# Optimization experiments

Hardware: AMD Instinct MI355X
Metric: run time of the kernel (lower is better)

## Reference

```python
import jax, jax.numpy as jnp
import numpy as np

N = 100_000      # nodes
E = 1_600_000    # edges (avg degree 16)
IN, H, OUT = 960, 192, 3
NB = 6           # block_num


def setup_inputs() -> dict:
    key = jax.random.key(0)
    ks = jax.random.split(key, 14)
    s = 0.05  # weight init scale
    x = jax.random.normal(ks[0], (N, IN), jnp.float32)
    src = jax.random.randint(ks[1], (E,), 0, N, jnp.int32)
    dst = jax.random.randint(ks[2], (E,), 0, N, jnp.int32)
    # normalized adjacency values (like D^-1 A entries)
    ew = jax.random.uniform(ks[3], (E,), jnp.float32) / 16.0
    w1 = jax.random.normal(ks[4], (IN, H), jnp.float32) * s
    l1 = jax.random.normal(ks[5], (IN, H), jnp.float32) * s
    b1 = jnp.zeros((H,), jnp.float32)
    wb = jax.random.normal(ks[6], (2 * NB, H, H), jnp.float32) * s
    lb = jax.random.normal(ks[7], (2 * NB, H, H), jnp.float32) * s
    bb = jnp.zeros((2 * NB, H), jnp.float32)
    w2 = jax.random.normal(ks[8], (H, OUT), jnp.float32) * s
    l2 = jax.random.normal(ks[9], (H, OUT), jnp.float32) * s
    b2 = jnp.zeros((OUT,), jnp.float32)
    return dict(x=x, src=src, dst=dst, ew=ew, w1=w1, l1=l1, b1=b1,
                wb=wb, lb=lb, bb=bb, w2=w2, l2=l2, b2=b2)


def reference(x, src, dst, ew, w1, l1, b1, wb, lb, bb, w2, l2, b2):
    def gcn(h, w, lw, b):
        # GraphConvolution: spmm(adj, h @ w) + h @ loop_w + b
        sup = h @ w                                   # [N, F_out]
        msg = sup[src] * ew[:, None]                  # gather + weight  [E, F_out]
        agg = jax.ops.segment_sum(msg, dst, num_segments=N)
        return agg + h @ lw + b

    h = gcn(x, w1, l1, b1)                            # conv1: in_dim -> hidden
    for i in range(NB):                               # GResBlocks
        a = gcn(h, wb[2 * i], lb[2 * i], bb[2 * i])
        a = gcn(a, wb[2 * i + 1], lb[2 * i + 1], bb[2 * i + 1])
        h = (h + a) * 0.5                             # residual scaling
    x_cat = h
    x_out = gcn(x_cat, w2, l2, b2)                    # conv2: hidden -> out_dim
    return (x_out, x_cat)
```

## Files before the change

kernel.cpp:

```cpp
#include <hip/hip_runtime.h>

typedef __attribute__((ext_vector_type(8))) short short8;
typedef __attribute__((ext_vector_type(4))) float f32x4;
typedef __attribute__((ext_vector_type(4))) int int4v;
typedef __attribute__((ext_vector_type(2))) unsigned int u32x2;

__device__ __forceinline__ float bf2f(unsigned short u) {
  return __uint_as_float(((unsigned)u) << 16);
}
__device__ __forceinline__ unsigned short f2bf(float f) {
  unsigned u = __float_as_uint(f);
  return (unsigned short)((u + 0x7FFFu + ((u >> 16) & 1u)) >> 16);
}

#define GLB_CAST(p) ((const __attribute__((address_space(1))) void*)(p))
#define LDS_CAST(p) ((__attribute__((address_space(3))) void*)(p))

__global__ void count_kernel(const int* __restrict__ dst, int* __restrict__ cnt, int E) {
  int e = blockIdx.x * blockDim.x + threadIdx.x;
  if (e < E) atomicAdd(&cnt[dst[e] + 1], 1);
}

__global__ __launch_bounds__(256) void scan_bsum_kernel(const int* __restrict__ cnt,
                                                        int* __restrict__ bsum, int n) {
  __shared__ int buf[256];
  int tid = threadIdx.x;
  int j0 = blockIdx.x * 1024 + tid * 4;
  int s = 0;
#pragma unroll
  for (int k = 0; k < 4; k++) {
    int j = j0 + k;
    if (j < n) s += cnt[j];
  }
  buf[tid] = s;
  __syncthreads();
  for (int off = 128; off > 0; off >>= 1) {
    if (tid < off) buf[tid] += buf[tid + off];
    __syncthreads();
  }
  if (tid == 0) bsum[blockIdx.x] = buf[0];
}

__global__ __launch_bounds__(256) void scan_small_kernel(const int* __restrict__ bsum,
                                                         int* __restrict__ boff, int nb) {
  __shared__ int buf[2][256];
  int tid = threadIdx.x;
  int C = (nb + 255) >> 8;
  int start = tid * C;
  int end = start + C; if (end > nb) end = nb;
  int s = 0;
  for (int j = start; j < end; j++) s += bsum[j];
  buf[0][tid] = s;
  __syncthreads();
  int pin = 0;
  for (int off = 1; off < 256; off <<= 1) {
    int v = buf[pin][tid];
    if (tid >= off) v += buf[pin][tid - off];
    buf[pin ^ 1][tid] = v;
    pin ^= 1;
    __syncthreads();
  }
  int run = (tid == 0) ? 0 : buf[pin][tid - 1];
  for (int j = start; j < end; j++) {
    boff[j] = run;
    run += bsum[j];
  }
}

__global__ __launch_bounds__(256) void scan_final_kernel(const int* __restrict__ cnt,
                                                         const int* __restrict__ boff,
                                                         int* __restrict__ rowptr,
                                                         int* __restrict__ cur,
                                                         int n, int nrows) {
  __shared__ int buf[2][256];
  int tid = threadIdx.x;
  int j0 = blockIdx.x * 1024 + tid * 4;
  int v[4];
  int s = 0;
#pragma unroll
  for (int k = 0; k < 4; k++) {
    int j = j0 + k;
    v[k] = (j < n) ? cnt[j] : 0;
    s += v[k];
  }
  buf[0][tid] = s;
  __syncthreads();
  int pin = 0;
  for (int off = 1; off < 256; off <<= 1) {
    int t = buf[pin][tid];
    if (tid >= off) t += buf[pin][tid - off];
    buf[pin ^ 1][tid] = t;
    pin ^= 1;
    __syncthreads();
  }
  int run = boff[blockIdx.x] + ((tid == 0) ? 0 : buf[pin][tid - 1]);
#pragma unroll
  for (int k = 0; k < 4; k++) {
    int j = j0 + k;
    if (j < n) {
      run += v[k];
      rowptr[j] = run;
      if (j < nrows) cur[j] = run;
    }
  }
}

__global__ void fill_kernel(const int* __restrict__ src, const int* __restrict__ dst,
                            const float* __restrict__ ew,
                            int* __restrict__ cur, int2* __restrict__ s_edge, int E) {
  int e = blockIdx.x * blockDim.x + threadIdx.x;
  if (e >= E) return;
  int r = dst[e];
  int pos = atomicAdd(&cur[r], 1);
  s_edge[pos] = make_int2(src[e], __float_as_int(ew[e]));
}

__global__ void prep_w_kernel(const float* __restrict__ w1,
                              const float* __restrict__ l1,
                              const float* __restrict__ wb,
                              const float* __restrict__ lb,
                              unsigned short* __restrict__ Wt1,
                              unsigned short* __restrict__ Wtb) {
  int tid = blockIdx.x * blockDim.x + threadIdx.x;
  const int n1 = 384 * 960;
  const int nb = 12 * 384 * 192;
  if (tid < n1) {
    int c = tid / 960, k = tid % 960;
    Wt1[tid] = f2bf((c < 192) ? w1[k * 192 + c] : l1[k * 192 + (c - 192)]);
  } else if (tid < n1 + nb) {
    int u = tid - n1;
    int i = u / (384 * 192);
    int r = u % (384 * 192);
    int c = r / 192, k = r % 192;
    Wtb[u] = f2bf((c < 192) ? wb[(i * 192 + k) * 192 + c]
                            : lb[(i * 192 + k) * 192 + (c - 192)]);
  }
}

__device__ __forceinline__ short8 cvt_f32x8(const float* p) {
  f32x4 a = *reinterpret_cast<const f32x4*>(p);
  f32x4 b = *reinterpret_cast<const f32x4*>(p + 4);
  short8 r;
  r[0] = (short)f2bf(a[0]); r[1] = (short)f2bf(a[1]);
  r[2] = (short)f2bf(a[2]); r[3] = (short)f2bf(a[3]);
  r[4] = (short)f2bf(b[0]); r[5] = (short)f2bf(b[1]);
  r[6] = (short)f2bf(b[2]); r[7] = (short)f2bf(b[3]);
  return r;
}

__global__ __launch_bounds__(512) void gemm_f32_kernel(const float* __restrict__ A,
                                                       const unsigned short* __restrict__ Wt,
                                                       unsigned short* __restrict__ out,
                                                       int nrows, int K) {
  __shared__ char lds_raw[40960];

  int tid = threadIdx.x;
  int lane = tid & 63;
  int w = tid >> 6;
  int rg = w >> 1, ch = w & 1;
  int row0blk = blockIdx.x * 256;
  int row0 = row0blk + rg * 64;
  int l15 = lane & 15, lq = lane >> 4;

  f32x4 acc[12][4];
#pragma unroll
  for (int cf = 0; cf < 12; cf++)
#pragma unroll
    for (int rf = 0; rf < 4; rf++) acc[cf][rf] = (f32x4)(0.0f);

  int tiles = K / 32;
  for (int tile = 0; tile < tiles; ++tile) {
    __syncthreads();
#pragma unroll
    for (int it = 0; it < 3; ++it) {
      int slot = it * 512 + tid;
      int q = slot / 384, c = slot - q * 384;
      const unsigned short* g = Wt + (size_t)c * K + tile * 32 + q * 8;
      __builtin_amdgcn_global_load_lds(GLB_CAST(g), LDS_CAST(lds_raw + 16384 + slot * 16), 16, 0, 0);
    }
#pragma unroll
    for (int it = 0; it < 2; ++it) {
      int slot = it * 512 + tid;
      int c = slot >> 8, row = slot & 255;
      int grow = row0blk + row;
      if (grow > nrows - 1) grow = nrows - 1;
      const float* g = A + (size_t)grow * K + tile * 32 + c * 8;
      *reinterpret_cast<short8*>(lds_raw + slot * 16) = cvt_f32x8(g);
    }
    __syncthreads();

    short8 af[4];
#pragma unroll
    for (int rf = 0; rf < 4; rf++)
      af[rf] = *reinterpret_cast<const short8*>(
          lds_raw + lq * 4096 + (rg * 64 + rf * 16 + l15) * 16);
#pragma unroll
    for (int cf = 0; cf < 12; cf++) {
      const short8 bf = *reinterpret_cast<const short8*>(
          lds_raw + 16384 + (lq * 384 + ch * 192 + cf * 16 + l15) * 16);
#pragma unroll
      for (int rf = 0; rf < 4; rf++)
        acc[cf][rf] = __builtin_amdgcn_mfma_f32_16x16x32_bf16(bf, af[rf], acc[cf][rf], 0, 0, 0);
    }
  }

#pragma unroll
  for (int rf = 0; rf < 4; rf++) {
    int row = row0 + rf * 16 + l15;
    if (row >= nrows) continue;
    unsigned short* orow = out + (size_t)row * 384 + ch * 192 + lq * 4;
#pragma unroll
    for (int cf = 0; cf < 12; cf++) {
      u32x2 pv;
      pv[0] = (unsigned)f2bf(acc[cf][rf][0]) | ((unsigned)f2bf(acc[cf][rf][1]) << 16);
      pv[1] = (unsigned)f2bf(acc[cf][rf][2]) | ((unsigned)f2bf(acc[cf][rf][3]) << 16);
      *reinterpret_cast<u32x2*>(orow + cf * 16) = pv;
    }
  }
}

__global__ __launch_bounds__(512) void gemm_bf16_db_kernel(const unsigned short* __restrict__ A,
                                                           const unsigned short* __restrict__ Wt,
                                                           unsigned short* __restrict__ out,
                                                           int nrows, int K) {
  extern __shared__ char lds_db[];

  int tid = threadIdx.x;
  int lane = tid & 63;
  int w = tid >> 6;
  int rg = w >> 1, ch = w & 1;
  int row0blk = blockIdx.x * 256;
  int row0 = row0blk + rg * 64;
  int l15 = lane & 15, lq = lane >> 4;

  f32x4 acc[12][4];
#pragma unroll
  for (int cf = 0; cf < 12; cf++)
#pragma unroll
    for (int rf = 0; rf < 4; rf++) acc[cf][rf] = (f32x4)(0.0f);

  auto stage = [&](int tile, int buf) {
    char* base = lds_db + buf * 40960;
#pragma unroll
    for (int it = 0; it < 3; ++it) {
      int slot = it * 512 + tid;
      int q = slot / 384, c = slot - q * 384;
      const unsigned short* g = Wt + (size_t)c * K + tile * 32 + q * 8;
      __builtin_amdgcn_global_load_lds(GLB_CAST(g), LDS_CAST(base + 16384 + slot * 16), 16, 0, 0);
    }
#pragma unroll
    for (int it = 0; it < 2; ++it) {
      int slot = it * 512 + tid;
      int c = slot >> 8, row = slot & 255;
      int grow = row0blk + row;
      if (grow > nrows - 1) grow = nrows - 1;
      const unsigned short* g = A + (size_t)grow * K + tile * 32 + c * 8;
      __builtin_amdgcn_global_load_lds(GLB_CAST(g), LDS_CAST(base + slot * 16), 16, 0, 0);
    }
  };

  int tiles = K / 32;
  stage(0, 0);
  __syncthreads();
  int cur = 0;
  for (int tile = 0; tile < tiles; ++tile) {
    if (tile + 1 < tiles) stage(tile + 1, cur ^ 1);
    char* base = lds_db + cur * 40960;
    short8 af[4];
#pragma unroll
    for (int rf = 0; rf < 4; rf++)
      af[rf] = *reinterpret_cast<const short8*>(
          base + lq * 4096 + (rg * 64 + rf * 16 + l15) * 16);
#pragma unroll
    for (int cf = 0; cf < 12; cf++) {
      const short8 bf = *reinterpret_cast<const short8*>(
          base + 16384 + (lq * 384 + ch * 192 + cf * 16 + l15) * 16);
#pragma unroll
      for (int rf = 0; rf < 4; rf++)
        acc[cf][rf] = __builtin_amdgcn_mfma_f32_16x16x32_bf16(bf, af[rf], acc[cf][rf], 0, 0, 0);
    }
    __syncthreads();
    cur ^= 1;
  }

#pragma unroll
  for (int rf = 0; rf < 4; rf++) {
    int row = row0 + rf * 16 + l15;
    if (row >= nrows) continue;
    unsigned short* orow = out + (size_t)row * 384 + ch * 192 + lq * 4;
#pragma unroll
    for (int cf = 0; cf < 12; cf++) {
      u32x2 pv;
      pv[0] = (unsigned)f2bf(acc[cf][rf][0]) | ((unsigned)f2bf(acc[cf][rf][1]) << 16);
      pv[1] = (unsigned)f2bf(acc[cf][rf][2]) | ((unsigned)f2bf(acc[cf][rf][3]) << 16);
      *reinterpret_cast<u32x2*>(orow + cf * 16) = pv;
    }
  }
}

__global__ __launch_bounds__(256) void spmm_kernel(const unsigned short* __restrict__ t,
                                                   const int* __restrict__ rowptr,
                                                   const int2* __restrict__ s_edge,
                                                   const float* __restrict__ bias,
                                                   const float* __restrict__ hprev32,
                                                   unsigned short* __restrict__ out16,
                                                   float* __restrict__ out32,
                                                   int n, int mode) {
  int tid = blockIdx.x * blockDim.x + threadIdx.x;
  int node = tid / 24;
  int c = tid % 24;
  if (node >= n) return;

  float acc[8];
#pragma unroll
  for (int j = 0; j < 8; j++) acc[j] = 0.0f;

  int e0 = rowptr[node], e1 = rowptr[node + 1];
  int e = e0;
  for (; e + 8 <= e1; e += 8) {
    int2 rec[8];
#pragma unroll
    for (int k = 0; k < 8; k++) rec[k] = s_edge[e + k];
    short8 v[8];
#pragma unroll
    for (int k = 0; k < 8; k++)
      v[k] = *reinterpret_cast<const short8*>(&t[(size_t)rec[k].x * 384 + c * 8]);
#pragma unroll
    for (int k = 0; k < 8; k++) {
      float wgt = __int_as_float(rec[k].y);
#pragma unroll
      for (int j = 0; j < 8; j++) acc[j] += wgt * bf2f((unsigned short)v[k][j]);
    }
  }
  for (; e + 2 <= e1; e += 2) {
    int2 ra = s_edge[e];
    int2 rb = s_edge[e + 1];
    float wa = __int_as_float(ra.y), wb = __int_as_float(rb.y);
    short8 va = *reinterpret_cast<const short8*>(&t[(size_t)ra.x * 384 + c * 8]);
    short8 vb = *reinterpret_cast<const short8*>(&t[(size_t)rb.x * 384 + c * 8]);
#pragma unroll
    for (int j = 0; j < 8; j++)
      acc[j] += wa * bf2f((unsigned short)va[j]) + wb * bf2f((unsigned short)vb[j]);
  }
  if (e < e1) {
    int2 ra = s_edge[e];
    float wa = __int_as_float(ra.y);
    short8 va = *reinterpret_cast<const short8*>(&t[(size_t)ra.x * 384 + c * 8]);
#pragma unroll
    for (int j = 0; j < 8; j++) acc[j] += wa * bf2f((unsigned short)va[j]);
  }

  short8 hlv = *reinterpret_cast<const short8*>(&t[(size_t)node * 384 + 192 + c * 8]);
  float r[8];
#pragma unroll
  for (int j = 0; j < 8; j++)
    r[j] = acc[j] + bf2f((unsigned short)hlv[j]) + bias[c * 8 + j];

  if (mode == 1) {
#pragma unroll
    for (int j = 0; j < 8; j++)
      r[j] = 0.5f * (hprev32[(size_t)node * 192 + c * 8 + j] + r[j]);
  }

  unsigned short o16[8];
#pragma unroll
  for (int j = 0; j < 8; j++) o16[j] = f2bf(r[j]);
  *reinterpret_cast<int4v*>(&out16[(size_t)node * 192 + c * 8]) =
      *reinterpret_cast<const int4v*>(o16);

  if (out32) {
    f32x4 lo, hi;
    lo[0] = r[0]; lo[1] = r[1]; lo[2] = r[2]; lo[3] = r[3];
    hi[0] = r[4]; hi[1] = r[5]; hi[2] = r[6]; hi[3] = r[7];
    *reinterpret_cast<f32x4*>(&out32[(size_t)node * 192 + c * 8]) = lo;
    *reinterpret_cast<f32x4*>(&out32[(size_t)node * 192 + c * 8 + 4]) = hi;
  }
}

__global__ __launch_bounds__(256) void conv2a_kernel(const float* __restrict__ h,
                                                     const float* __restrict__ w2,
                                                     const float* __restrict__ l2,
                                                     const float* __restrict__ b2,
                                                     float* __restrict__ sup2,
                                                     float* __restrict__ hl2, int n) {
  int wid = (blockIdx.x * blockDim.x + threadIdx.x) >> 6;
  int lane = threadIdx.x & 63;
  if (wid >= n) return;
  float sa[3] = {0.f, 0.f, 0.f}, sl[3] = {0.f, 0.f, 0.f};
  for (int k = lane; k < 192; k += 64) {
    float hv = h[(size_t)wid * 192 + k];
#pragma unroll
    for (int j = 0; j < 3; j++) {
      sa[j] += hv * w2[k * 3 + j];
      sl[j] += hv * l2[k * 3 + j];
    }
  }
#pragma unroll
  for (int j = 0; j < 3; j++) {
    for (int off = 32; off > 0; off >>= 1) {
      sa[j] += __shfl_down(sa[j], off);
      sl[j] += __shfl_down(sl[j], off);
    }
  }
  if (lane == 0) {
#pragma unroll
    for (int j = 0; j < 3; j++) {
      sup2[(size_t)wid * 3 + j] = sa[j];
      hl2[(size_t)wid * 3 + j] = sl[j] + b2[j];
    }
  }
}

__global__ __launch_bounds__(256) void conv2b_kernel(const int* __restrict__ rowptr,
                                                     const int2* __restrict__ s_edge,
                                                     const float* __restrict__ sup2,
                                                     const float* __restrict__ hl2,
                                                     float* __restrict__ out, int n) {
  int node = blockIdx.x * blockDim.x + threadIdx.x;
  if (node >= n) return;
  float acc[3] = {0.f, 0.f, 0.f};
  int e0 = rowptr[node], e1 = rowptr[node + 1];
  for (int e = e0; e < e1; e++) {
    int2 rec = s_edge[e];
    float wgt = __int_as_float(rec.y);
#pragma unroll
    for (int j = 0; j < 3; j++) acc[j] += wgt * sup2[(size_t)rec.x * 3 + j];
  }
#pragma unroll
  for (int j = 0; j < 3; j++)
    out[(size_t)node * 3 + j] = acc[j] + hl2[(size_t)node * 3 + j];
}

extern "C" void kernel_launch(void* const* d_in, const int* in_sizes, int n_in,
                              void* d_out, int out_size, void* d_ws, size_t ws_size,
                              hipStream_t stream) {
  const float* x  = (const float*)d_in[0];
  const int* src  = (const int*)d_in[1];
  const int* dst  = (const int*)d_in[2];
  const float* ew = (const float*)d_in[3];
  const float* w1 = (const float*)d_in[4];
  const float* l1 = (const float*)d_in[5];
  const float* b1 = (const float*)d_in[6];
  const float* wb = (const float*)d_in[7];
  const float* lb = (const float*)d_in[8];
  const float* bb = (const float*)d_in[9];
  const float* w2 = (const float*)d_in[10];
  const float* l2 = (const float*)d_in[11];
  const float* b2 = (const float*)d_in[12];
  float* out = (float*)d_out;

  const int N = in_sizes[0] / 960;
  const int E = in_sizes[1];

  float* h32 = out + (size_t)N * 3;

  char* p = (char*)d_ws;
  auto alloc = [&](size_t bytes) {
    char* q = p;
    p += (bytes + 255) & ~(size_t)255;
    return q;
  };
  unsigned short* Wt1 = (unsigned short*)alloc((size_t)384 * 960 * 2);
  unsigned short* Wtb = (unsigned short*)alloc((size_t)12 * 384 * 192 * 2);
  unsigned short* t   = (unsigned short*)alloc((size_t)N * 384 * 2);
  unsigned short* h16 = (unsigned short*)alloc((size_t)N * 192 * 2);
  unsigned short* a16 = (unsigned short*)alloc((size_t)N * 192 * 2);
  int* rowptr = (int*)alloc((size_t)(N + 1) * 4);
  int* cur    = (int*)alloc((size_t)N * 4);
  int* cnt    = (int*)alloc((size_t)(N + 1) * 4);
  int* bsum   = (int*)alloc((size_t)1024 * 4);
  int* boff   = (int*)alloc((size_t)1024 * 4);
  int2* s_edge = (int2*)alloc((size_t)E * 8);
  float* sup2 = (float*)alloc((size_t)N * 3 * 4);
  float* hl2  = (float*)alloc((size_t)N * 3 * 4);
  if ((size_t)(p - (char*)d_ws) > ws_size) return;

  const int nScan = N + 1;
  const int nBlk = (nScan + 1023) / 1024;

  hipMemsetAsync(cnt, 0, (size_t)(N + 1) * 4, stream);
  count_kernel<<<(E + 255) / 256, 256, 0, stream>>>(dst, cnt, E);
  scan_bsum_kernel<<<nBlk, 256, 0, stream>>>(cnt, bsum, nScan);
  scan_small_kernel<<<1, 256, 0, stream>>>(bsum, boff, nBlk);
  scan_final_kernel<<<nBlk, 256, 0, stream>>>(cnt, boff, rowptr, cur, nScan, N);
  fill_kernel<<<(E + 255) / 256, 256, 0, stream>>>(src, dst, ew, cur, s_edge, E);
  {
    int total = 384 * 960 + 12 * 384 * 192;
    prep_w_kernel<<<(total + 255) / 256, 256, 0, stream>>>(w1, l1, wb, lb, Wt1, Wtb);
  }

  int gBlocks = (N + 255) / 256;
  int sBlocks = (N * 24 + 255) / 256;
  const int DB_LDS = 81920;

  gemm_f32_kernel<<<gBlocks, 512, 0, stream>>>(x, Wt1, t, N, 960);
  spmm_kernel<<<sBlocks, 256, 0, stream>>>(t, rowptr, s_edge, b1,
                                           (const float*)nullptr, h16, h32, N, 0);

  for (int i = 0; i < 12; i += 2) {
    gemm_bf16_db_kernel<<<gBlocks, 512, DB_LDS, stream>>>(
        h16, Wtb + (size_t)i * 384 * 192, t, N, 192);
    spmm_kernel<<<sBlocks, 256, 0, stream>>>(t, rowptr, s_edge, bb + (size_t)i * 192,
                                             (const float*)nullptr, a16, (float*)nullptr, N, 0);
    gemm_bf16_db_kernel<<<gBlocks, 512, DB_LDS, stream>>>(
        a16, Wtb + (size_t)(i + 1) * 384 * 192, t, N, 192);
    spmm_kernel<<<sBlocks, 256, 0, stream>>>(t, rowptr, s_edge, bb + (size_t)(i + 1) * 192,
                                             h32, h16, h32, N, 1);
  }

  conv2a_kernel<<<(N + 3) / 4, 256, 0, stream>>>(h32, w2, l2, b2, sup2, hl2, N);
  conv2b_kernel<<<(N + 255) / 256, 256, 0, stream>>>(rowptr, s_edge, sup2, hl2, out, N);
}
```

Before: 2.528 ms.

## Restructure SpMM to 8 lanes per node with shuffled edge records and bf16 residual

The SpMM kernel now gives each node 8 lanes instead of 24, and each lane covers three 64-column slices. One coalesced edge-record load per 8 edges is spread across the lanes with shuffles, and more row gathers are kept in flight per thread. The fp32 residual copy is dropped: the residual now reads bf16 h16, and h32 is produced once at the end by a small conversion kernel. This cuts per-layer fp32 read/write traffic, but keeps the residual stream at bf16 precision, which may add accumulation error.

Result: faster. 2.469 ms (-2.3%).

```diff
diff --git a/kernel.cpp b/kernel.cpp
--- a/kernel.cpp
+++ b/kernel.cpp
@@ -137,9 +137,7 @@
   }
 }
 
-__device__ __forceinline__ short8 cvt_f32x8(const float* p) {
-  f32x4 a = *reinterpret_cast<const f32x4*>(p);
-  f32x4 b = *reinterpret_cast<const f32x4*>(p + 4);
+__device__ __forceinline__ short8 cvt_pair(f32x4 a, f32x4 b) {
   short8 r;
   r[0] = (short)f2bf(a[0]); r[1] = (short)f2bf(a[1]);
   r[2] = (short)f2bf(a[2]); r[3] = (short)f2bf(a[3]);
@@ -185,7 +183,9 @@
       int grow = row0blk + row;
       if (grow > nrows - 1) grow = nrows - 1;
       const float* g = A + (size_t)grow * K + tile * 32 + c * 8;
-      *reinterpret_cast<short8*>(lds_raw + slot * 16) = cvt_f32x8(g);
+      f32x4 a0 = *reinterpret_cast<const f32x4*>(g);
+      f32x4 a1 = *reinterpret_cast<const f32x4*>(g + 4);
+      *reinterpret_cast<short8*>(lds_raw + slot * 16) = cvt_pair(a0, a1);
     }
     __syncthreads();
 
@@ -302,82 +302,99 @@
                                                    const int* __restrict__ rowptr,
                                                    const int2* __restrict__ s_edge,
                                                    const float* __restrict__ bias,
-                                                   const float* __restrict__ hprev32,
+                                                   const unsigned short* __restrict__ hprev16,
                                                    unsigned short* __restrict__ out16,
-                                                   float* __restrict__ out32,
                                                    int n, int mode) {
   int tid = blockIdx.x * blockDim.x + threadIdx.x;
-  int node = tid / 24;
-  int c = tid % 24;
+  int node = tid >> 3;
+  int sub = tid & 7;
   if (node >= n) return;
-
-  float acc[8];
-#pragma unroll
-  for (int j = 0; j < 8; j++) acc[j] = 0.0f;
+  int co = sub * 8;
+
+  float acc[3][8];
+#pragma unroll
+  for (int q = 0; q < 3; q++)
+#pragma unroll
+    for (int j = 0; j < 8; j++) acc[q][j] = 0.0f;
 
   int e0 = rowptr[node], e1 = rowptr[node + 1];
-  int e = e0;
-  for (; e + 8 <= e1; e += 8) {
-    int2 rec[8];
-#pragma unroll
-    for (int k = 0; k < 8; k++) rec[k] = s_edge[e + k];
-    short8 v[8];
-#pragma unroll
-    for (int k = 0; k < 8; k++)
-      v[k] = *reinterpret_cast<const short8*>(&t[(size_t)rec[k].x * 384 + c * 8]);
-#pragma unroll
-    for (int k = 0; k < 8; k++) {
-      float wgt = __int_as_float(rec[k].y);
-#pragma unroll
-      for (int j = 0; j < 8; j++) acc[j] += wgt * bf2f((unsigned short)v[k][j]);
-    }
-  }
-  for (; e + 2 <= e1; e += 2) {
-    int2 ra = s_edge[e];
-    int2 rb = s_edge[e + 1];
-    float wa = __int_as_float(ra.y), wb = __int_as_float(rb.y);
-    short8 va = *reinterpret_cast<const short8*>(&t[(size_t)ra.x * 384 + c * 8]);
-    short8 vb = *reinterpret_cast<const short8*>(&t[(size_t)rb.x * 384 + c * 8]);
+  int ne = e1 - e0;
+  int base = 0;
+  for (; base + 8 <= ne; base += 8) {
+    int2 rec = s_edge[e0 + base + sub];
+#pragma unroll
+    for (int half = 0; half < 2; half++) {
+      short8 v[4][3];
+      float wgt[4];
+#pragma unroll
+      for (int k = 0; k < 4; k++) {
+        int kk = half * 4 + k;
+        int sn = __shfl(rec.x, kk, 8);
+        wgt[k] = __int_as_float(__shfl(rec.y, kk, 8));
+        const unsigned short* row = t + (size_t)sn * 384;
+#pragma unroll
+        for (int q = 0; q < 3; q++)
+          v[k][q] = *reinterpret_cast<const short8*>(row + q * 64 + co);
+      }
+#pragma unroll
+      for (int k = 0; k < 4; k++)
+#pragma unroll
+        for (int q = 0; q < 3; q++)
+#pragma unroll
+          for (int j = 0; j < 8; j++)
+            acc[q][j] += wgt[k] * bf2f((unsigned short)v[k][q][j]);
+    }
+  }
+  for (; base < ne; base++) {
+    int2 rec = s_edge[e0 + base];
+    float wgt = __int_as_float(rec.y);
+    const unsigned short* row = t + (size_t)rec.x * 384;
+#pragma unroll
+    for (int q = 0; q < 3; q++) {
+      short8 v = *reinterpret_cast<const short8*>(row + q * 64 + co);
+#pragma unroll
+      for (int j = 0; j < 8; j++) acc[q][j] += wgt * bf2f((unsigned short)v[j]);
+    }
+  }
+
+  const unsigned short* hlrow = t + (size_t)node * 384 + 192;
+#pragma unroll
+  for (int q = 0; q < 3; q++) {
+    short8 hlv = *reinterpret_cast<const short8*>(hlrow + q * 64 + co);
+    float r[8];
 #pragma unroll
     for (int j = 0; j < 8; j++)
-      acc[j] += wa * bf2f((unsigned short)va[j]) + wb * bf2f((unsigned short)vb[j]);
-  }
-  if (e < e1) {
-    int2 ra = s_edge[e];
-    float wa = __int_as_float(ra.y);
-    short8 va = *reinterpret_cast<const short8*>(&t[(size_t)ra.x * 384 + c * 8]);
-#pragma unroll
-    for (int j = 0; j < 8; j++) acc[j] += wa * bf2f((unsigned short)va[j]);
-  }
-
-  short8 hlv = *reinterpret_cast<const short8*>(&t[(size_t)node * 384 + 192 + c * 8]);
-  float r[8];
-#pragma unroll
-  for (int j = 0; j < 8; j++)
-    r[j] = acc[j] + bf2f((unsigned short)hlv[j]) + bias[c * 8 + j];
-
-  if (mode == 1) {
-#pragma unroll
-    for (int j = 0; j < 8; j++)
-      r[j] = 0.5f * (hprev32[(size_t)node * 192 + c * 8 + j] + r[j]);
-  }
-
-  unsigned short o16[8];
-#pragma unroll
-  for (int j = 0; j < 8; j++) o16[j] = f2bf(r[j]);
-  *reinterpret_cast<int4v*>(&out16[(size_t)node * 192 + c * 8]) =
-      *reinterpret_cast<const int4v*>(o16);
-
-  if (out32) {
-    f32x4 lo, hi;
-    lo[0] = r[0]; lo[1] = r[1]; lo[2] = r[2]; lo[3] = r[3];
-    hi[0] = r[4]; hi[1] = r[5]; hi[2] = r[6]; hi[3] = r[7];
-    *reinterpret_cast<f32x4*>(&out32[(size_t)node * 192 + c * 8]) = lo;
-    *reinterpret_cast<f32x4*>(&out32[(size_t)node * 192 + c * 8 + 4]) = hi;
-  }
-}
-
-__global__ __launch_bounds__(256) void conv2a_kernel(const float* __restrict__ h,
+      r[j] = acc[q][j] + bf2f((unsigned short)hlv[j]) + bias[q * 64 + co + j];
+    if (mode == 1) {
+      short8 hp = *reinterpret_cast<const short8*>(&hprev16[(size_t)node * 192 + q * 64 + co]);
+#pragma unroll
+      for (int j = 0; j < 8; j++)
+        r[j] = 0.5f * (bf2f((unsigned short)hp[j]) + r[j]);
+    }
+    unsigned short o16[8];
+#pragma unroll
+    for (int j = 0; j < 8; j++) o16[j] = f2bf(r[j]);
+    *reinterpret_cast<int4v*>(&out16[(size_t)node * 192 + q * 64 + co]) =
+        *reinterpret_cast<const int4v*>(o16);
+  }
+}
+
+__global__ __launch_bounds__(256) void cvt_kernel(const unsigned short* __restrict__ h16,
+                                                  float* __restrict__ h32, int n8) {
+  int i = blockIdx.x * blockDim.x + threadIdx.x;
+  if (i >= n8) return;
+  short8 v = *reinterpret_cast<const short8*>(&h16[(size_t)i * 8]);
+  f32x4 lo, hi;
+#pragma unroll
+  for (int j = 0; j < 4; j++) {
+    lo[j] = bf2f((unsigned short)v[j]);
+    hi[j] = bf2f((unsigned short)v[4 + j]);
+  }
+  *reinterpret_cast<f32x4*>(&h32[(size_t)i * 8]) = lo;
+  *reinterpret_cast<f32x4*>(&h32[(size_t)i * 8 + 4]) = hi;
+}
+
+__global__ __launch_bounds__(256) void conv2a_kernel(const unsigned short* __restrict__ h,
                                                      const float* __restrict__ w2,
                                                      const float* __restrict__ l2,
                                                      const float* __restrict__ b2,
@@ -388,7 +405,7 @@
   if (wid >= n) return;
   float sa[3] = {0.f, 0.f, 0.f}, sl[3] = {0.f, 0.f, 0.f};
   for (int k = lane; k < 192; k += 64) {
-    float hv = h[(size_t)wid * 192 + k];
+    float hv = bf2f(h[(size_t)wid * 192 + k]);
 #pragma unroll
     for (int j = 0; j < 3; j++) {
       sa[j] += hv * w2[k * 3 + j];
@@ -490,24 +507,26 @@
   }
 
   int gBlocks = (N + 255) / 256;
-  int sBlocks = (N * 24 + 255) / 256;
+  int sBlocks = (N * 8 + 255) / 256;
   const int DB_LDS = 81920;
 
   gemm_f32_kernel<<<gBlocks, 512, 0, stream>>>(x, Wt1, t, N, 960);
   spmm_kernel<<<sBlocks, 256, 0, stream>>>(t, rowptr, s_edge, b1,
-                                           (const float*)nullptr, h16, h32, N, 0);
+                                           (const unsigned short*)nullptr, h16, N, 0);
 
   for (int i = 0; i < 12; i += 2) {
     gemm_bf16_db_kernel<<<gBlocks, 512, DB_LDS, stream>>>(
         h16, Wtb + (size_t)i * 384 * 192, t, N, 192);
     spmm_kernel<<<sBlocks, 256, 0, stream>>>(t, rowptr, s_edge, bb + (size_t)i * 192,
-                                             (const float*)nullptr, a16, (float*)nullptr, N, 0);
+                                             (const unsigned short*)nullptr, a16, N, 0);
     gemm_bf16_db_kernel<<<gBlocks, 512, DB_LDS, stream>>>(
         a16, Wtb + (size_t)(i + 1) * 384 * 192, t, N, 192);
     spmm_kernel<<<sBlocks, 256, 0, stream>>>(t, rowptr, s_edge, bb + (size_t)(i + 1) * 192,
-                                             h32, h16, h32, N, 1);
-  }
-
-  conv2a_kernel<<<(N + 3) / 4, 256, 0, stream>>>(h32, w2, l2, b2, sup2, hl2, N);
+                                             h16, h16, N, 1);
+  }
+
+  cvt_kernel<<<(N * 24 + 255) / 256, 256, 0, stream>>>(h16, h32, N * 24);
+
+  conv2a_kernel<<<(N + 3) / 4, 256, 0, stream>>>(h16, w2, l2, b2, sup2, hl2, N);
   conv2b_kernel<<<(N + 255) / 256, 256, 0, stream>>>(rowptr, s_edge, sup2, hl2, out, N);
 }
```
